# Kernel optimization log

Measured on AMD Instinct MI355X. Metric: run time of the kernel, lower is better.

The kernel has to match this reference:

```python
import jax, jax.numpy as jnp
import numpy as np

NEG_BIG = -9e15

def setup_inputs() -> dict:
    key = jax.random.key(0)
    k1, k2, k3, k4, k5 = jax.random.split(key, 5)
    B, N, Fin, Fout = 32768, 15, 128, 128
    x = jax.random.normal(k1, (B, N, Fin), dtype=jnp.float32)
    adj = jax.random.randint(k2, (B, N, N), 0, 2, dtype=jnp.int32)
    W = jax.random.normal(k3, (Fin, Fout), dtype=jnp.float32) * (1.414 / np.sqrt(Fin))
    a_src = jax.random.normal(k4, (Fout,), dtype=jnp.float32) * 0.1
    a_dst = jax.random.normal(k5, (Fout,), dtype=jnp.float32) * 0.1
    return {"x": x, "adj": adj, "W": W, "a_src": a_src, "a_dst": a_dst}

def reference(x, adj, W, a_src, a_dst):
    alpha = 0.2  # leaky relu negative slope
    h = jnp.einsum('bnf,fo->bno', x, W)            # [B,N,Fout]
    s_src = jnp.einsum('bno,o->bn', h, a_src)      # contribution of node i
    s_dst = jnp.einsum('bno,o->bn', h, a_dst)      # contribution of node j
    # e[b,i,j] = leakyrelu(a . concat(h_i, h_j))
    e = jax.nn.leaky_relu(s_src[:, :, None] + s_dst[:, None, :], negative_slope=alpha)
    att = jnp.where(adj > 0, e, NEG_BIG)
    # NOTE: original applies softmax over dim=1 (the i axis), faithfully reproduced
    att = jax.nn.softmax(att, axis=1)
    # dropout skipped (eval mode)
    h_prime = jax.nn.elu(jnp.einsum('bij,bjo->bio', att, h))
    return h_prime
```

## Files before the change

### kernel.cpp

```cpp
#include <hip/hip_runtime.h>
#include <hip/hip_bf16.h>

typedef __attribute__((ext_vector_type(4))) float f32x4;
typedef __attribute__((ext_vector_type(8))) short short8;
typedef __attribute__((ext_vector_type(4))) _Float16 f16x4;

__device__ __forceinline__ short f2bf(float f) {
    unsigned u = __builtin_bit_cast(unsigned, f);
    u += 0x7fffu + ((u >> 16) & 1u);
    return (short)(unsigned short)(u >> 16);
}

__global__ void gat_pre(const float* __restrict__ W, const float* __restrict__ a_src,
                        const float* __restrict__ a_dst, unsigned short* __restrict__ wt,
                        float* __restrict__ wa) {
    int blk = blockIdx.x, t = threadIdx.x;
    if (blk < 8) {
        int e = blk * 256 + t;
        int kk = e >> 9, ct = (e >> 6) & 7, lane = e & 63;
        int lq = lane >> 4, l15 = lane & 15;
        short8 v;
#pragma unroll
        for (int jj = 0; jj < 8; ++jj)
            v[jj] = f2bf(W[(kk * 32 + lq * 8 + jj) * 128 + ct * 16 + l15]);
        *(short8*)(wt + (size_t)e * 8) = v;
    } else if (t < 128) {
        float s1 = 0.f, s2 = 0.f;
        for (int o = 0; o < 128; ++o) {
            float w = W[t * 128 + o];
            s1 += w * a_src[o];
            s2 += w * a_dst[o];
        }
        wa[t] = s1; wa[128 + t] = s2;
    }
}

__global__ __launch_bounds__(256, 4) void gat_main(
    const float* __restrict__ x, const int* __restrict__ adj,
    const unsigned short* __restrict__ wfrag, const float* __restrict__ wa,
    float* __restrict__ out, int B)
{
    __shared__ __align__(16) unsigned short wlds[16384];
    __shared__ __align__(16) float walds[256];

    const int t = threadIdx.x;
    const int wv = t >> 6;
    const int lane = t & 63;
    const int lq = lane >> 4, l15 = lane & 15;

#pragma unroll
    for (int i = 0; i < 8; ++i)
        *(float4*)((char*)wlds + (t + 256 * i) * 16) =
            *(const float4*)((const char*)wfrag + (t + 256 * i) * 16);
    if (t < 64) *(float4*)(walds + t * 4) = *(const float4*)(wa + t * 4);
    __syncthreads();

    const int wid = blockIdx.x * 4 + wv;
    const int wstride = gridDim.x * 4;
    const f32x4 z4 = {0.f, 0.f, 0.f, 0.f};
    const bool vrow = (l15 < 15);

    for (int b = wid; b < B; b += wstride) {
        f32x4 a[8];
        {
            const float* xb = x + (size_t)b * 1920 + l15 * 128 + lq * 8;
#pragma unroll
            for (int kk = 0; kk < 4; ++kk) {
                a[2 * kk]     = vrow ? *(const f32x4*)(xb + kk * 32)     : z4;
                a[2 * kk + 1] = vrow ? *(const f32x4*)(xb + kk * 32 + 4) : z4;
            }
        }
        int a4;
        {
            const int* ab = adj + (size_t)b * 225 + l15 * 15 + lq * 4;
            int v0 = vrow ? ab[0] : 0;
            int v1 = vrow ? ab[1] : 0;
            int v2 = vrow ? ab[2] : 0;
            int v3 = (vrow && lq < 3) ? ab[3] : 0;
            a4 = (v0 ? 1 : 0) | (v1 ? 2 : 0) | (v2 ? 4 : 0) | (v3 ? 8 : 0);
        }

        float ps = 0.f, pd = 0.f;
        short8 af[4];
#pragma unroll
        for (int kk = 0; kk < 4; ++kk) {
            f32x4 a0 = a[2 * kk], a1 = a[2 * kk + 1];
            const float* wb = walds + kk * 32 + lq * 8;
            f32x4 s0 = *(const f32x4*)(wb);
            f32x4 s1 = *(const f32x4*)(wb + 4);
            f32x4 d0 = *(const f32x4*)(wb + 128);
            f32x4 d1 = *(const f32x4*)(wb + 132);
            ps += a0.x * s0.x + a0.y * s0.y + a0.z * s0.z + a0.w * s0.w
                + a1.x * s1.x + a1.y * s1.y + a1.z * s1.z + a1.w * s1.w;
            pd += a0.x * d0.x + a0.y * d0.y + a0.z * d0.z + a0.w * d0.w
                + a1.x * d1.x + a1.y * d1.y + a1.z * d1.z + a1.w * d1.w;
            union { unsigned u[4]; short8 s8; } cv;
            asm("v_cvt_pk_bf16_f32 %0, %1, %2" : "=v"(cv.u[0]) : "v"(a0.x), "v"(a0.y));
            asm("v_cvt_pk_bf16_f32 %0, %1, %2" : "=v"(cv.u[1]) : "v"(a0.z), "v"(a0.w));
            asm("v_cvt_pk_bf16_f32 %0, %1, %2" : "=v"(cv.u[2]) : "v"(a1.x), "v"(a1.y));
            asm("v_cvt_pk_bf16_f32 %0, %1, %2" : "=v"(cv.u[3]) : "v"(a1.z), "v"(a1.w));
            af[kk] = cv.s8;
        }

        float ss = ps + __shfl_xor(ps, 16);
        ss += __shfl_xor(ss, 32);
        float sd = pd + __shfl_xor(pd, 16);
        sd += __shfl_xor(sd, 32);

        f32x4 acc[8];
#pragma unroll
        for (int ct = 0; ct < 8; ++ct) acc[ct] = z4;
#pragma unroll
        for (int kk = 0; kk < 4; ++kk) {
#pragma unroll
            for (int ct = 0; ct < 8; ++ct) {
                short8 bf = *(const short8*)(wlds + ((size_t)(kk * 8 + ct) * 64 + lane) * 8);
                acc[ct] = __builtin_amdgcn_mfma_f32_16x16x32_bf16(af[kk], bf, acc[ct], 0, 0, 0);
            }
        }

        float attv[4];
#pragma unroll
        for (int r = 0; r < 4; ++r) {
            float sdj = __shfl(sd, lq * 4 + r);
            float e = ss + sdj;
            e = e > 0.f ? e : 0.2f * e;
            e = fminf(e, 30.f);
            float pexp = ((a4 >> r) & 1) ? __expf(e) : 1e-26f;
            if (l15 == 15) pexp = 0.f;
            float sm = pexp;
            sm += __shfl_xor(sm, 1);
            sm += __shfl_xor(sm, 2);
            sm += __shfl_xor(sm, 4);
            sm += __shfl_xor(sm, 8);
            attv[r] = pexp * __builtin_amdgcn_rcpf(sm);
        }

        f16x4 attf;
        attf[0] = (_Float16)attv[0]; attf[1] = (_Float16)attv[1];
        attf[2] = (_Float16)attv[2]; attf[3] = (_Float16)attv[3];
        f32x4 dq[8];
#pragma unroll
        for (int ct = 0; ct < 8; ++ct) {
            f16x4 hA;
            hA[0] = (_Float16)acc[ct][0]; hA[1] = (_Float16)acc[ct][1];
            hA[2] = (_Float16)acc[ct][2]; hA[3] = (_Float16)acc[ct][3];
            f32x4 o4 = __builtin_amdgcn_mfma_f32_16x16x16f16(hA, attf, z4, 0, 0, 0);
#pragma unroll
            for (int r = 0; r < 4; ++r) {
                float u = o4[r];
                o4[r] = u > 0.f ? u : (__expf(u) - 1.f);
            }
            dq[ct] = o4;
        }

        {
            float* const orow = out + (size_t)b * 1920 + l15 * 128 + lq * 4;
            if (vrow) {
#pragma unroll
                for (int ct = 0; ct < 8; ++ct)
                    *(f32x4*)(orow + ct * 16) = dq[ct];
            }
        }
    }
}

extern "C" void kernel_launch(void* const* d_in, const int* in_sizes, int n_in,
                              void* d_out, int out_size, void* d_ws, size_t ws_size,
                              hipStream_t stream) {
    const float* x     = (const float*)d_in[0];
    const int*   adj   = (const int*)d_in[1];
    const float* W     = (const float*)d_in[2];
    const float* a_src = (const float*)d_in[3];
    const float* a_dst = (const float*)d_in[4];
    float* out = (float*)d_out;

    unsigned short* wt = (unsigned short*)d_ws;
    float* wa = (float*)((char*)d_ws + 32768);

    int B = in_sizes[0] / (15 * 128);
    int nblk = 2048;

    gat_pre<<<9, 256, 0, stream>>>(W, a_src, a_dst, wt, wa);
    gat_main<<<nblk, 256, 0, stream>>>(x, adj, wt, wa, out, B);
}
```

Before: 138.4 us.

## Software-pipeline batch loads: prefetch next graph's x and adj during compute

Restructures the per-wave batch loop so the next graph's x rows and adjacency mask are loaded into registers while the current graph's MFMA, softmax and output stores run. The bf16 conversion and score dot products for the next graph are done after the stores. This hides global load latency inside each wave. It costs extra registers, so launch bounds drop to 3 blocks per CU and the grid is halved to 1024 blocks. The loop now runs B / wstride iterations, which drops any leftover graphs when B is not a multiple of the wave count. It also assumes every wave has at least one graph.

```diff
diff --git a/kernel.cpp b/kernel.cpp
--- a/kernel.cpp
+++ b/kernel.cpp
@@ -35,7 +35,51 @@
     }
 }
 
-__global__ __launch_bounds__(256, 4) void gat_main(
+__device__ __forceinline__ void load_batch(const float* __restrict__ x,
+                                           const int* __restrict__ adj,
+                                           int b, int lq, int l15,
+                                           f32x4 (&xv)[8], int& am) {
+    const f32x4 z4 = {0.f, 0.f, 0.f, 0.f};
+    const bool vrow = (l15 < 15);
+    const float* xb = x + (size_t)b * 1920 + l15 * 128 + lq * 8;
+#pragma unroll
+    for (int kk = 0; kk < 4; ++kk) {
+        xv[2 * kk]     = vrow ? *(const f32x4*)(xb + kk * 32)     : z4;
+        xv[2 * kk + 1] = vrow ? *(const f32x4*)(xb + kk * 32 + 4) : z4;
+    }
+    const int* ab = adj + (size_t)b * 225 + l15 * 15 + lq * 4;
+    int v0 = vrow ? ab[0] : 0;
+    int v1 = vrow ? ab[1] : 0;
+    int v2 = vrow ? ab[2] : 0;
+    int v3 = (vrow && lq < 3) ? ab[3] : 0;
+    am = (v0 ? 1 : 0) | (v1 ? 2 : 0) | (v2 ? 4 : 0) | (v3 ? 8 : 0);
+}
+
+__device__ __forceinline__ void prep(const f32x4 (&xv)[8], const float* __restrict__ walds,
+                                     int lq, float& ps, float& pd, short8 (&af)[4]) {
+    ps = 0.f; pd = 0.f;
+#pragma unroll
+    for (int kk = 0; kk < 4; ++kk) {
+        f32x4 a0 = xv[2 * kk], a1 = xv[2 * kk + 1];
+        const float* wb = walds + kk * 32 + lq * 8;
+        f32x4 s0 = *(const f32x4*)(wb);
+        f32x4 s1 = *(const f32x4*)(wb + 4);
+        f32x4 d0 = *(const f32x4*)(wb + 128);
+        f32x4 d1 = *(const f32x4*)(wb + 132);
+        ps += a0.x * s0.x + a0.y * s0.y + a0.z * s0.z + a0.w * s0.w
+            + a1.x * s1.x + a1.y * s1.y + a1.z * s1.z + a1.w * s1.w;
+        pd += a0.x * d0.x + a0.y * d0.y + a0.z * d0.z + a0.w * d0.w
+            + a1.x * d1.x + a1.y * d1.y + a1.z * d1.z + a1.w * d1.w;
+        union { unsigned u[4]; short8 s8; } cv;
+        asm("v_cvt_pk_bf16_f32 %0, %1, %2" : "=v"(cv.u[0]) : "v"(a0.x), "v"(a0.y));
+        asm("v_cvt_pk_bf16_f32 %0, %1, %2" : "=v"(cv.u[1]) : "v"(a0.z), "v"(a0.w));
+        asm("v_cvt_pk_bf16_f32 %0, %1, %2" : "=v"(cv.u[2]) : "v"(a1.x), "v"(a1.y));
+        asm("v_cvt_pk_bf16_f32 %0, %1, %2" : "=v"(cv.u[3]) : "v"(a1.z), "v"(a1.w));
+        af[kk] = cv.s8;
+    }
+}
+
+__global__ __launch_bounds__(256, 3) void gat_main(
     const float* __restrict__ x, const int* __restrict__ adj,
     const unsigned short* __restrict__ wfrag, const float* __restrict__ wa,
     float* __restrict__ out, int B)
@@ -57,50 +101,22 @@
 
     const int wid = blockIdx.x * 4 + wv;
     const int wstride = gridDim.x * 4;
+    const int niter = B / wstride;
     const f32x4 z4 = {0.f, 0.f, 0.f, 0.f};
     const bool vrow = (l15 < 15);
 
-    for (int b = wid; b < B; b += wstride) {
-        f32x4 a[8];
-        {
-            const float* xb = x + (size_t)b * 1920 + l15 * 128 + lq * 8;
-#pragma unroll
-            for (int kk = 0; kk < 4; ++kk) {
-                a[2 * kk]     = vrow ? *(const f32x4*)(xb + kk * 32)     : z4;
-                a[2 * kk + 1] = vrow ? *(const f32x4*)(xb + kk * 32 + 4) : z4;
-            }
-        }
-        int a4;
-        {
-            const int* ab = adj + (size_t)b * 225 + l15 * 15 + lq * 4;
-            int v0 = vrow ? ab[0] : 0;
-            int v1 = vrow ? ab[1] : 0;
-            int v2 = vrow ? ab[2] : 0;
-            int v3 = (vrow && lq < 3) ? ab[3] : 0;
-            a4 = (v0 ? 1 : 0) | (v1 ? 2 : 0) | (v2 ? 4 : 0) | (v3 ? 8 : 0);
-        }
-
-        float ps = 0.f, pd = 0.f;
-        short8 af[4];
-#pragma unroll
-        for (int kk = 0; kk < 4; ++kk) {
-            f32x4 a0 = a[2 * kk], a1 = a[2 * kk + 1];
-            const float* wb = walds + kk * 32 + lq * 8;
-            f32x4 s0 = *(const f32x4*)(wb);
-            f32x4 s1 = *(const f32x4*)(wb + 4);
-            f32x4 d0 = *(const f32x4*)(wb + 128);
-            f32x4 d1 = *(const f32x4*)(wb + 132);
-            ps += a0.x * s0.x + a0.y * s0.y + a0.z * s0.z + a0.w * s0.w
-                + a1.x * s1.x + a1.y * s1.y + a1.z * s1.z + a1.w * s1.w;
-            pd += a0.x * d0.x + a0.y * d0.y + a0.z * d0.z + a0.w * d0.w
-                + a1.x * d1.x + a1.y * d1.y + a1.z * d1.z + a1.w * d1.w;
-            union { unsigned u[4]; short8 s8; } cv;
-            asm("v_cvt_pk_bf16_f32 %0, %1, %2" : "=v"(cv.u[0]) : "v"(a0.x), "v"(a0.y));
-            asm("v_cvt_pk_bf16_f32 %0, %1, %2" : "=v"(cv.u[1]) : "v"(a0.z), "v"(a0.w));
-            asm("v_cvt_pk_bf16_f32 %0, %1, %2" : "=v"(cv.u[2]) : "v"(a1.x), "v"(a1.y));
-            asm("v_cvt_pk_bf16_f32 %0, %1, %2" : "=v"(cv.u[3]) : "v"(a1.z), "v"(a1.w));
-            af[kk] = cv.s8;
-        }
+    f32x4 xr[8];
+    int a4 = 0, am2 = 0;
+    short8 af[4];
+    float ps = 0.f, pd = 0.f;
+
+    load_batch(x, adj, wid, lq, l15, xr, a4);
+    prep(xr, walds, lq, ps, pd, af);
+
+    for (int i = 0; i < niter; ++i) {
+        const int b = wid + i * wstride;
+
+        if (i + 1 < niter) load_batch(x, adj, b + wstride, lq, l15, xr, am2);
 
         float ss = ps + __shfl_xor(ps, 16);
         ss += __shfl_xor(ss, 32);
@@ -162,6 +178,11 @@
                     *(f32x4*)(orow + ct * 16) = dq[ct];
             }
         }
+
+        if (i + 1 < niter) {
+            prep(xr, walds, lq, ps, pd, af);
+            a4 = am2;
+        }
     }
 }
 
@@ -179,7 +200,7 @@
     float* wa = (float*)((char*)d_ws + 32768);
 
     int B = in_sizes[0] / (15 * 128);
-    int nblk = 2048;
+    int nblk = 1024;
 
     gat_pre<<<9, 256, 0, stream>>>(W, a_src, a_dst, wt, wa);
     gat_main<<<nblk, 256, 0, stream>>>(x, adj, wt, wa, out, B);
```

Result: slower. 349.2 us (+152.4%).
